# Optimization experiments

Hardware: AMD Instinct MI355X
Metric: run time of the kernel (lower is better)

Reference implementation:

```python
import jax, jax.numpy as jnp
import numpy as np

GROUPS = 32
EPS = 1e-5
NUM_HEADS = 8

def group_norm(x, w, b):
    # x: [B, C, H, W], normalize over (C//G, H, W) per group
    B, C, H, W = x.shape
    xg = x.reshape(B, GROUPS, C // GROUPS, H, W)
    mean = xg.mean(axis=(2, 3, 4), keepdims=True)
    var = xg.var(axis=(2, 3, 4), keepdims=True)
    xg = (xg - mean) * jax.lax.rsqrt(var + EPS)
    x = xg.reshape(B, C, H, W)
    return x * w[None, :, None, None] + b[None, :, None, None]

def setup_inputs() -> dict:
    key = jax.random.key(0)
    ks = jax.random.split(key, 3)
    C = 512
    x = jax.random.normal(ks[0], (8, C, 32, 32), dtype=jnp.float32)
    gn_w = jnp.ones((C,), jnp.float32)
    gn_b = jnp.zeros((C,), jnp.float32)
    # 1x1 conv weights stored as [out, in] matrices
    qkv_w = jax.random.normal(ks[1], (3 * C, C), dtype=jnp.float32) * (C ** -0.5)
    qkv_b = jnp.zeros((3 * C,), jnp.float32)
    proj_w = jax.random.normal(ks[2], (C, C), dtype=jnp.float32) * (C ** -0.5)
    proj_b = jnp.zeros((C,), jnp.float32)
    return {"x": x, "gn_w": gn_w, "gn_b": gn_b, "qkv_w": qkv_w,
            "qkv_b": qkv_b, "proj_w": proj_w, "proj_b": proj_b}

def reference(x, gn_w, gn_b, qkv_w, qkv_b, proj_w, proj_b):
    B, C, H, W = x.shape
    nh = NUM_HEADS
    hd = C // nh
    N = H * W
    residual = x
    xn = group_norm(x, gn_w, gn_b)
    # 1x1 conv == channel matmul: [B, 3C, H, W]
    qkv = jnp.einsum('bchw,oc->bohw', xn, qkv_w) + qkv_b[None, :, None, None]
    # [B, 3, nh, hd, N] -> q/k/v each [B, nh, N, hd]
    qkv = qkv.reshape(B, 3, nh, hd, N).transpose(1, 0, 2, 4, 3)
    q, k, v = qkv[0], qkv[1], qkv[2]
    scale = hd ** -0.5
    attn = jnp.einsum('bhqd,bhkd->bhqk', q, k) * scale
    attn = jax.nn.softmax(attn, axis=-1)
    out = jnp.einsum('bhqk,bhkd->bhqd', attn, v)  # [B, nh, N, hd]
    out = out.transpose(0, 1, 3, 2).reshape(B, C, H, W)
    out = jnp.einsum('bchw,oc->bohw', out, proj_w) + proj_b[None, :, None, None]
    return out + residual
```

## Files before the change

kernel.cpp:

```cpp
#include <hip/hip_runtime.h>


typedef __bf16 bf16;
typedef __bf16 bf16x8 __attribute__((ext_vector_type(8)));
typedef __bf16 bf16x4 __attribute__((ext_vector_type(4)));
typedef float  f32x4  __attribute__((ext_vector_type(4)));

#define MFMA_16x16x32(A, B, C) __builtin_amdgcn_mfma_f32_16x16x32_bf16((A), (B), (C), 0, 0, 0)

static __device__ __forceinline__ void async_stage_128x32(
    const bf16* __restrict__ g0, bf16* lds, int tid) {
  const int wv = tid >> 6, ln = tid & 63;
#pragma unroll
  for (int cc = 0; cc < 2; ++cc) {
    const int c = wv + cc * 4;
    const bf16* g = g0 + (size_t)(c * 16 + (ln >> 2)) * 512 + (ln & 3) * 8;
    __builtin_amdgcn_global_load_lds(
        (const __attribute__((address_space(1))) void*)g,
        (__attribute__((address_space(3))) void*)(lds + c * 512),
        16, 0, 0);
  }
}

__global__ void wconv_kernel(const float* __restrict__ qw, const float* __restrict__ pw,
                             bf16* __restrict__ wq, bf16* __restrict__ wp) {
  const int i = blockIdx.x * 256 + threadIdx.x;
  if (i < 1536 * 512) wq[i] = (bf16)qw[i];
  if (i < 512 * 512)  wp[i] = (bf16)pw[i];
}

__global__ void gn_stats_kernel(const float* __restrict__ x,
                                float* __restrict__ meanp, float* __restrict__ rstdp) {
  const int bg = blockIdx.x;
  const float4* p = (const float4*)(x + (size_t)bg * 16384);
  float s = 0.f, s2 = 0.f;
#pragma unroll 4
  for (int i = threadIdx.x; i < 4096; i += 256) {
    float4 v = p[i];
    s  += (v.x + v.y) + (v.z + v.w);
    s2 += (v.x * v.x + v.y * v.y) + (v.z * v.z + v.w * v.w);
  }
#pragma unroll
  for (int d = 1; d < 64; d <<= 1) {
    s  += __shfl_xor(s,  d);
    s2 += __shfl_xor(s2, d);
  }
  __shared__ float as[4], as2[4];
  if ((threadIdx.x & 63) == 0) { as[threadIdx.x >> 6] = s; as2[threadIdx.x >> 6] = s2; }
  __syncthreads();
  if (threadIdx.x == 0) {
    float S  = as[0] + as[1] + as[2] + as[3];
    float S2 = as2[0] + as2[1] + as2[2] + as2[3];
    float m = S * (1.0f / 16384.0f);
    float v = S2 * (1.0f / 16384.0f) - m * m;
    meanp[bg] = m;
    rstdp[bg] = rsqrtf(v + 1e-5f);
  }
}

__global__ void gn_apply_kernel(const float* __restrict__ x,
                                const float* __restrict__ gn_w, const float* __restrict__ gn_b,
                                const float* __restrict__ meanp, const float* __restrict__ rstdp,
                                bf16* __restrict__ xn_t) {
  const int n0 = blockIdx.x * 64, c0 = blockIdx.y * 64, b = blockIdx.z;
  __shared__ float tile[64 * 68];
  const int t = threadIdx.x;
  const float* xb = x + ((size_t)b * 512 + c0) * 1024 + n0;
#pragma unroll
  for (int i = 0; i < 4; ++i) {
    int idx = t + i * 256;
    int cl  = idx >> 4;
    int n4  = (idx & 15) * 4;
    float4 v = *(const float4*)(xb + (size_t)cl * 1024 + n4);
    int c  = c0 + cl;
    int bg = b * 32 + (c >> 4);
    float sc = rstdp[bg] * gn_w[c];
    float sh = gn_b[c] - meanp[bg] * sc;
    tile[(n4 + 0) * 68 + cl] = v.x * sc + sh;
    tile[(n4 + 1) * 68 + cl] = v.y * sc + sh;
    tile[(n4 + 2) * 68 + cl] = v.z * sc + sh;
    tile[(n4 + 3) * 68 + cl] = v.w * sc + sh;
  }
  __syncthreads();
  bf16* ob = xn_t + ((size_t)b * 1024 + n0) * 512 + c0;
#pragma unroll
  for (int i = 0; i < 16; ++i) {
    int idx = t + i * 256;
    int nl = idx >> 6, cl = idx & 63;
    ob[(size_t)nl * 512 + cl] = (bf16)tile[nl * 68 + cl];
  }
}

__global__ __launch_bounds__(256) void qkv_gemm_kernel(
    const bf16* __restrict__ W, const bf16* __restrict__ xn_t,
    const float* __restrict__ qkv_b, bf16* __restrict__ qkv_t,
    bf16* __restrict__ v_t) {
  const int n0 = blockIdx.x * 128;
  const int o0 = blockIdx.y * 128;
  const int b  = blockIdx.z;
  __shared__ bf16 As[128 * 32];
  __shared__ bf16 Bs[128 * 32];
  const int tid = threadIdx.x, ln = tid & 63, wv = tid >> 6;
  const int mw = (wv >> 1) * 64, nw = (wv & 1) * 64;
  const int l15 = ln & 15, lg = ln >> 4;
  const bf16* gA = W + (size_t)o0 * 512;
  const bf16* gB = xn_t + ((size_t)b * 1024 + n0) * 512;
  f32x4 acc[4][4] = {};
  for (int kk = 0; kk < 512; kk += 32) {
    async_stage_128x32(gA + kk, As, tid);
    async_stage_128x32(gB + kk, Bs, tid);
    __syncthreads();
    bf16x8 af[4], bfr[4];
#pragma unroll
    for (int mi = 0; mi < 4; ++mi)
      af[mi] = *(const bf16x8*)(&As[(mw + mi * 16 + l15) * 32 + lg * 8]);
#pragma unroll
    for (int nj = 0; nj < 4; ++nj)
      bfr[nj] = *(const bf16x8*)(&Bs[(nw + nj * 16 + l15) * 32 + lg * 8]);
#pragma unroll
    for (int mi = 0; mi < 4; ++mi)
#pragma unroll
      for (int nj = 0; nj < 4; ++nj)
        acc[mi][nj] = MFMA_16x16x32(af[mi], bfr[nj], acc[mi][nj]);
    __syncthreads();
  }
  if (o0 < 1024) {
#pragma unroll
    for (int mi = 0; mi < 4; ++mi) {
      const int o = o0 + mw + mi * 16 + lg * 4;
      const float b0 = qkv_b[o], b1 = qkv_b[o + 1], b2 = qkv_b[o + 2], b3 = qkv_b[o + 3];
#pragma unroll
      for (int nj = 0; nj < 4; ++nj) {
        const int n = n0 + nw + nj * 16 + l15;
        f32x4 v = acc[mi][nj];
        bf16x4 st = { (bf16)(v.x + b0), (bf16)(v.y + b1), (bf16)(v.z + b2), (bf16)(v.w + b3) };
        *(bf16x4*)(&qkv_t[((size_t)b * 1024 + n) * 1536 + o]) = st;
      }
    }
  } else {
#pragma unroll
    for (int mi = 0; mi < 4; ++mi) {
      const int o  = o0 + mw + mi * 16 + lg * 4;
      const int hd = o - 1024;
      const float b0 = qkv_b[o], b1 = qkv_b[o + 1], b2 = qkv_b[o + 2], b3 = qkv_b[o + 3];
      bf16* vb = v_t + ((size_t)b * 512 + hd) * 1024;
#pragma unroll
      for (int nj = 0; nj < 4; ++nj) {
        const int n = n0 + nw + nj * 16 + l15;
        f32x4 v = acc[mi][nj];
        vb[0 * 1024 + n] = (bf16)(v.x + b0);
        vb[1 * 1024 + n] = (bf16)(v.y + b1);
        vb[2 * 1024 + n] = (bf16)(v.z + b2);
        vb[3 * 1024 + n] = (bf16)(v.w + b3);
      }
    }
  }
}

__global__ __launch_bounds__(256) void attn_kernel(
    const bf16* __restrict__ qkv_t, const bf16* __restrict__ v_t,
    bf16* __restrict__ at_t) {
  const int qt = blockIdx.x;
  const int b  = blockIdx.y >> 3;
  const int h  = blockIdx.y & 7;
  __shared__ bf16 Kt[64 * 72];
  __shared__ bf16 Vt[64 * 72];
  __shared__ bf16 Pw[4 * 64 * 72];
  const int tid = threadIdx.x, ln = tid & 63, wv = tid >> 6;
  const int l15 = ln & 15, g = ln >> 4;
  const bf16* hq  = qkv_t + (size_t)b * 1024 * 1536 + h * 64;
  const bf16* hk  = hq + 512;
  const bf16* vtb = v_t + (size_t)(b * 8 + h) * 64 * 1024;
  bf16* Pme = &Pw[wv * 64 * 72];

  const int qb = qt * 256 + wv * 64;
  bf16x8 qf[4][2];
#pragma unroll
  for (int m = 0; m < 4; ++m)
#pragma unroll
    for (int ks = 0; ks < 2; ++ks)
      qf[m][ks] = *(const bf16x8*)(hq + (size_t)(qb + m * 16 + l15) * 1536 + ks * 32 + g * 8);

  f32x4 oacc[4][4] = {};
  float mst[4], lst[4];
#pragma unroll
  for (int m = 0; m < 4; ++m) { mst[m] = -1e30f; lst[m] = 0.f; }

  const int srow = tid >> 2, scg = (tid & 3) * 16;
  bf16x8 kpre0 = *(const bf16x8*)(hk + (size_t)srow * 1536 + scg);
  bf16x8 kpre1 = *(const bf16x8*)(hk + (size_t)srow * 1536 + scg + 8);
  bf16x8 vpre0 = *(const bf16x8*)(vtb + (size_t)srow * 1024 + scg);
  bf16x8 vpre1 = *(const bf16x8*)(vtb + (size_t)srow * 1024 + scg + 8);

  for (int kt = 0; kt < 16; ++kt) {
    __syncthreads();
    *(bf16x8*)(&Kt[srow * 72 + scg])     = kpre0;
    *(bf16x8*)(&Kt[srow * 72 + scg + 8]) = kpre1;
    *(bf16x8*)(&Vt[srow * 72 + scg])     = vpre0;
    *(bf16x8*)(&Vt[srow * 72 + scg + 8]) = vpre1;
    __syncthreads();
    if (kt < 15) {
      const bf16* hk2  = hk  + (size_t)((kt + 1) * 64 + srow) * 1536 + scg;
      const bf16* vtb2 = vtb + (size_t)srow * 1024 + (kt + 1) * 64 + scg;
      kpre0 = *(const bf16x8*)(hk2);
      kpre1 = *(const bf16x8*)(hk2 + 8);
      vpre0 = *(const bf16x8*)(vtb2);
      vpre1 = *(const bf16x8*)(vtb2 + 8);
    }

    bf16x8 kf[4][2];
#pragma unroll
    for (int kj = 0; kj < 4; ++kj)
#pragma unroll
      for (int ks = 0; ks < 2; ++ks)
        kf[kj][ks] = *(const bf16x8*)(&Kt[(kj * 16 + l15) * 72 + ks * 32 + g * 8]);

    float alpha[4];
#pragma unroll
    for (int m = 0; m < 4; ++m) {
      f32x4 st[4] = {};
#pragma unroll
      for (int ks = 0; ks < 2; ++ks)
#pragma unroll
        for (int kj = 0; kj < 4; ++kj)
          st[kj] = MFMA_16x16x32(kf[kj][ks], qf[m][ks], st[kj]);
#pragma unroll
      for (int kj = 0; kj < 4; ++kj)
#pragma unroll
        for (int r = 0; r < 4; ++r) st[kj][r] *= 0.125f;
      float mx = st[0][0];
#pragma unroll
      for (int kj = 0; kj < 4; ++kj)
#pragma unroll
        for (int r = 0; r < 4; ++r) mx = fmaxf(mx, st[kj][r]);
      mx = fmaxf(mx, __shfl_xor(mx, 16));
      mx = fmaxf(mx, __shfl_xor(mx, 32));
      const float mnew = fmaxf(mst[m], mx);
      alpha[m] = __expf(mst[m] - mnew);
      mst[m] = mnew;
      float rsum = 0.f;
#pragma unroll
      for (int kj = 0; kj < 4; ++kj) {
        float e0 = __expf(st[kj][0] - mnew);
        float e1 = __expf(st[kj][1] - mnew);
        float e2 = __expf(st[kj][2] - mnew);
        float e3 = __expf(st[kj][3] - mnew);
        rsum += (e0 + e1) + (e2 + e3);
        bf16x4 pe = { (bf16)e0, (bf16)e1, (bf16)e2, (bf16)e3 };
        *(bf16x4*)(&Pme[(m * 16 + l15) * 72 + kj * 16 + g * 4]) = pe;
      }
      lst[m] = lst[m] * alpha[m] + rsum;
#pragma unroll
      for (int dt = 0; dt < 4; ++dt)
#pragma unroll
        for (int r = 0; r < 4; ++r) oacc[m][dt][r] *= alpha[m];
    }

#pragma unroll
    for (int ks = 0; ks < 2; ++ks) {
      bf16x8 vf[4];
#pragma unroll
      for (int dt = 0; dt < 4; ++dt)
        vf[dt] = *(const bf16x8*)(&Vt[(dt * 16 + l15) * 72 + ks * 32 + g * 8]);
#pragma unroll
      for (int m = 0; m < 4; ++m) {
        bf16x8 pf = *(const bf16x8*)(&Pme[(m * 16 + l15) * 72 + ks * 32 + g * 8]);
#pragma unroll
        for (int dt = 0; dt < 4; ++dt)
          oacc[m][dt] = MFMA_16x16x32(vf[dt], pf, oacc[m][dt]);
      }
    }
  }

#pragma unroll
  for (int m = 0; m < 4; ++m) {
    float l = lst[m];
    l += __shfl_xor(l, 16);
    l += __shfl_xor(l, 32);
    const float inv = 1.0f / l;
    const int q = qb + m * 16 + l15;
#pragma unroll
    for (int dt = 0; dt < 4; ++dt) {
      bf16x4 ov = { (bf16)(oacc[m][dt][0] * inv), (bf16)(oacc[m][dt][1] * inv),
                    (bf16)(oacc[m][dt][2] * inv), (bf16)(oacc[m][dt][3] * inv) };
      *(bf16x4*)(&at_t[((size_t)b * 1024 + q) * 512 + h * 64 + dt * 16 + g * 4]) = ov;
    }
  }
}

__global__ __launch_bounds__(256) void proj_gemm_kernel(
    const bf16* __restrict__ at_t, const bf16* __restrict__ wp,
    const float* __restrict__ proj_b, const float* __restrict__ x,
    float* __restrict__ out) {
  const int i0 = blockIdx.x * 128;
  const int c0 = blockIdx.y * 128;
  const int b  = blockIdx.z;
  __shared__ bf16 As[128 * 32];
  __shared__ bf16 Bs[128 * 32];
  const int tid = threadIdx.x, ln = tid & 63, wv = tid >> 6;
  const int mw = (wv >> 1) * 64, nw = (wv & 1) * 64;
  const int l15 = ln & 15, lg = ln >> 4;
  const bf16* gA = at_t + ((size_t)b * 1024 + i0) * 512;
  const bf16* gB = wp + (size_t)c0 * 512;
  f32x4 acc[4][4] = {};
  for (int kk = 0; kk < 512; kk += 32) {
    async_stage_128x32(gA + kk, As, tid);
    async_stage_128x32(gB + kk, Bs, tid);
    __syncthreads();
    bf16x8 af[4], bfr[4];
#pragma unroll
    for (int mi = 0; mi < 4; ++mi)
      af[mi] = *(const bf16x8*)(&As[(mw + mi * 16 + l15) * 32 + lg * 8]);
#pragma unroll
    for (int nj = 0; nj < 4; ++nj)
      bfr[nj] = *(const bf16x8*)(&Bs[(nw + nj * 16 + l15) * 32 + lg * 8]);
#pragma unroll
    for (int mi = 0; mi < 4; ++mi)
#pragma unroll
      for (int nj = 0; nj < 4; ++nj)
        acc[mi][nj] = MFMA_16x16x32(af[mi], bfr[nj], acc[mi][nj]);
    __syncthreads();
  }
#pragma unroll
  for (int mi = 0; mi < 4; ++mi) {
    const int i = i0 + mw + mi * 16 + lg * 4;
#pragma unroll
    for (int nj = 0; nj < 4; ++nj) {
      const int c = c0 + nw + nj * 16 + l15;
      const float bias = proj_b[c];
      const size_t off = ((size_t)b * 512 + c) * 1024 + i;
      const float4 res = *(const float4*)(x + off);
      f32x4 v = acc[mi][nj];
      float4 ov;
      ov.x = v.x + bias + res.x;
      ov.y = v.y + bias + res.y;
      ov.z = v.z + bias + res.z;
      ov.w = v.w + bias + res.w;
      *(float4*)(out + off) = ov;
    }
  }
}

extern "C" void kernel_launch(void* const* d_in, const int* in_sizes, int n_in,
                              void* d_out, int out_size, void* d_ws, size_t ws_size,
                              hipStream_t stream) {
  (void)in_sizes; (void)n_in; (void)out_size; (void)ws_size;
  const float* x      = (const float*)d_in[0];
  const float* gn_w   = (const float*)d_in[1];
  const float* gn_b   = (const float*)d_in[2];
  const float* qkv_w  = (const float*)d_in[3];
  const float* qkv_b  = (const float*)d_in[4];
  const float* proj_w = (const float*)d_in[5];
  const float* proj_b = (const float*)d_in[6];
  float* out = (float*)d_out;

  char* ws = (char*)d_ws;
  float* meanp = (float*)ws;
  float* rstdp = meanp + 256;
  bf16* wq    = (bf16*)(ws + 4096);
  bf16* wp    = wq + (size_t)1536 * 512;
  bf16* xn_t  = wp + (size_t)512 * 512;
  bf16* qkv_t = xn_t + (size_t)8 * 1024 * 512;
  bf16* at_t  = qkv_t + (size_t)8 * 1024 * 1536;
  bf16* v_t   = at_t + (size_t)8 * 1024 * 512;

  hipLaunchKernelGGL(wconv_kernel,    dim3(3072),      dim3(256), 0, stream, qkv_w, proj_w, wq, wp);
  hipLaunchKernelGGL(gn_stats_kernel, dim3(256),       dim3(256), 0, stream, x, meanp, rstdp);
  hipLaunchKernelGGL(gn_apply_kernel, dim3(16, 8, 8),  dim3(256), 0, stream, x, gn_w, gn_b, meanp, rstdp, xn_t);
  hipLaunchKernelGGL(qkv_gemm_kernel, dim3(8, 12, 8),  dim3(256), 0, stream, wq, xn_t, qkv_b, qkv_t, v_t);
  hipLaunchKernelGGL(attn_kernel,     dim3(4, 64),     dim3(256), 0, stream, qkv_t, v_t, at_t);
  hipLaunchKernelGGL(proj_gemm_kernel,dim3(8, 4, 8),   dim3(256), 0, stream, at_t, wp, proj_b, x, out);
}
```

Measured before the change: 174.1 us.

## Split attention KV range across two wave groups and fold softmax scale into Q

The attention kernel now uses 512-thread blocks over twice as many query tiles. Each block's waves split into two halves, each processing half of the key/value sequence with 32 queries per wave, and the partial results are merged through LDS using a log-sum-exp combine. The 1/sqrt(d) scale is applied to Q in the QKV GEMM epilogue rather than to every score tile. The intent is more parallel blocks and fewer registers per wave, so the 256 workgroups fill the GPU better, at the cost of extra LDS traffic and a final merge step.

```diff
diff --git a/kernel.cpp b/kernel.cpp
--- a/kernel.cpp
+++ b/kernel.cpp
@@ -125,6 +125,7 @@
     __syncthreads();
   }
   if (o0 < 1024) {
+    const float qs = (o0 < 512) ? 0.125f : 1.0f;
 #pragma unroll
     for (int mi = 0; mi < 4; ++mi) {
       const int o = o0 + mw + mi * 16 + lg * 4;
@@ -133,7 +134,8 @@
       for (int nj = 0; nj < 4; ++nj) {
         const int n = n0 + nw + nj * 16 + l15;
         f32x4 v = acc[mi][nj];
-        bf16x4 st = { (bf16)(v.x + b0), (bf16)(v.y + b1), (bf16)(v.z + b2), (bf16)(v.w + b3) };
+        bf16x4 st = { (bf16)((v.x + b0) * qs), (bf16)((v.y + b1) * qs),
+                      (bf16)((v.z + b2) * qs), (bf16)((v.w + b3) * qs) };
         *(bf16x4*)(&qkv_t[((size_t)b * 1024 + n) * 1536 + o]) = st;
       }
     }
@@ -157,51 +159,53 @@
   }
 }
 
-__global__ __launch_bounds__(256) void attn_kernel(
+__global__ __launch_bounds__(512, 4) void attn_kernel(
     const bf16* __restrict__ qkv_t, const bf16* __restrict__ v_t,
     bf16* __restrict__ at_t) {
   const int qt = blockIdx.x;
   const int b  = blockIdx.y >> 3;
   const int h  = blockIdx.y & 7;
-  __shared__ bf16 Kt[64 * 72];
-  __shared__ bf16 Vt[64 * 72];
-  __shared__ bf16 Pw[4 * 64 * 72];
+  __shared__ __align__(16) char smem[73728];
   const int tid = threadIdx.x, ln = tid & 63, wv = tid >> 6;
+  const int half = wv >> 2, w4 = wv & 3;
   const int l15 = ln & 15, g = ln >> 4;
+  bf16* Kt = (bf16*)(smem + half * 18432);
+  bf16* Vt = Kt + 64 * 72;
+  bf16* Pme = (bf16*)(smem + 36864) + wv * 32 * 72;
   const bf16* hq  = qkv_t + (size_t)b * 1024 * 1536 + h * 64;
   const bf16* hk  = hq + 512;
   const bf16* vtb = v_t + (size_t)(b * 8 + h) * 64 * 1024;
-  bf16* Pme = &Pw[wv * 64 * 72];
-
-  const int qb = qt * 256 + wv * 64;
-  bf16x8 qf[4][2];
-#pragma unroll
-  for (int m = 0; m < 4; ++m)
+
+  const int qb = qt * 128 + w4 * 32;
+  bf16x8 qf[2][2];
+#pragma unroll
+  for (int m = 0; m < 2; ++m)
 #pragma unroll
     for (int ks = 0; ks < 2; ++ks)
       qf[m][ks] = *(const bf16x8*)(hq + (size_t)(qb + m * 16 + l15) * 1536 + ks * 32 + g * 8);
 
-  f32x4 oacc[4][4] = {};
-  float mst[4], lst[4];
-#pragma unroll
-  for (int m = 0; m < 4; ++m) { mst[m] = -1e30f; lst[m] = 0.f; }
-
-  const int srow = tid >> 2, scg = (tid & 3) * 16;
-  bf16x8 kpre0 = *(const bf16x8*)(hk + (size_t)srow * 1536 + scg);
-  bf16x8 kpre1 = *(const bf16x8*)(hk + (size_t)srow * 1536 + scg + 8);
-  bf16x8 vpre0 = *(const bf16x8*)(vtb + (size_t)srow * 1024 + scg);
-  bf16x8 vpre1 = *(const bf16x8*)(vtb + (size_t)srow * 1024 + scg + 8);
-
-  for (int kt = 0; kt < 16; ++kt) {
+  f32x4 oacc[2][4] = {};
+  float mst[2] = { -1e30f, -1e30f }, lst[2] = { 0.f, 0.f };
+
+  const int t256 = tid & 255;
+  const int srow = t256 >> 2, scg = (t256 & 3) * 16;
+  const int kt0 = half * 8;
+  bf16x8 kpre0 = *(const bf16x8*)(hk + (size_t)(kt0 * 64 + srow) * 1536 + scg);
+  bf16x8 kpre1 = *(const bf16x8*)(hk + (size_t)(kt0 * 64 + srow) * 1536 + scg + 8);
+  bf16x8 vpre0 = *(const bf16x8*)(vtb + (size_t)srow * 1024 + kt0 * 64 + scg);
+  bf16x8 vpre1 = *(const bf16x8*)(vtb + (size_t)srow * 1024 + kt0 * 64 + scg + 8);
+
+  for (int i = 0; i < 8; ++i) {
     __syncthreads();
     *(bf16x8*)(&Kt[srow * 72 + scg])     = kpre0;
     *(bf16x8*)(&Kt[srow * 72 + scg + 8]) = kpre1;
     *(bf16x8*)(&Vt[srow * 72 + scg])     = vpre0;
     *(bf16x8*)(&Vt[srow * 72 + scg + 8]) = vpre1;
     __syncthreads();
-    if (kt < 15) {
-      const bf16* hk2  = hk  + (size_t)((kt + 1) * 64 + srow) * 1536 + scg;
-      const bf16* vtb2 = vtb + (size_t)srow * 1024 + (kt + 1) * 64 + scg;
+    if (i < 7) {
+      const int ktn = kt0 + i + 1;
+      const bf16* hk2  = hk  + (size_t)(ktn * 64 + srow) * 1536 + scg;
+      const bf16* vtb2 = vtb + (size_t)srow * 1024 + ktn * 64 + scg;
       kpre0 = *(const bf16x8*)(hk2);
       kpre1 = *(const bf16x8*)(hk2 + 8);
       vpre0 = *(const bf16x8*)(vtb2);
@@ -215,19 +219,14 @@
       for (int ks = 0; ks < 2; ++ks)
         kf[kj][ks] = *(const bf16x8*)(&Kt[(kj * 16 + l15) * 72 + ks * 32 + g * 8]);
 
-    float alpha[4];
-#pragma unroll
-    for (int m = 0; m < 4; ++m) {
+#pragma unroll
+    for (int m = 0; m < 2; ++m) {
       f32x4 st[4] = {};
 #pragma unroll
       for (int ks = 0; ks < 2; ++ks)
 #pragma unroll
         for (int kj = 0; kj < 4; ++kj)
           st[kj] = MFMA_16x16x32(kf[kj][ks], qf[m][ks], st[kj]);
-#pragma unroll
-      for (int kj = 0; kj < 4; ++kj)
-#pragma unroll
-        for (int r = 0; r < 4; ++r) st[kj][r] *= 0.125f;
       float mx = st[0][0];
 #pragma unroll
       for (int kj = 0; kj < 4; ++kj)
@@ -235,8 +234,8 @@
         for (int r = 0; r < 4; ++r) mx = fmaxf(mx, st[kj][r]);
       mx = fmaxf(mx, __shfl_xor(mx, 16));
       mx = fmaxf(mx, __shfl_xor(mx, 32));
-      const float mnew = fmaxf(mst[m], mx);
-      alpha[m] = __expf(mst[m] - mnew);
+      const float mnew  = fmaxf(mst[m], mx);
+      const float alpha = __expf(mst[m] - mnew);
       mst[m] = mnew;
       float rsum = 0.f;
 #pragma unroll
@@ -249,11 +248,11 @@
         bf16x4 pe = { (bf16)e0, (bf16)e1, (bf16)e2, (bf16)e3 };
         *(bf16x4*)(&Pme[(m * 16 + l15) * 72 + kj * 16 + g * 4]) = pe;
       }
-      lst[m] = lst[m] * alpha[m] + rsum;
+      lst[m] = lst[m] * alpha + rsum;
 #pragma unroll
       for (int dt = 0; dt < 4; ++dt)
 #pragma unroll
-        for (int r = 0; r < 4; ++r) oacc[m][dt][r] *= alpha[m];
+        for (int r = 0; r < 4; ++r) oacc[m][dt][r] *= alpha;
     }
 
 #pragma unroll
@@ -263,7 +262,7 @@
       for (int dt = 0; dt < 4; ++dt)
         vf[dt] = *(const bf16x8*)(&Vt[(dt * 16 + l15) * 72 + ks * 32 + g * 8]);
 #pragma unroll
-      for (int m = 0; m < 4; ++m) {
+      for (int m = 0; m < 2; ++m) {
         bf16x8 pf = *(const bf16x8*)(&Pme[(m * 16 + l15) * 72 + ks * 32 + g * 8]);
 #pragma unroll
         for (int dt = 0; dt < 4; ++dt)
@@ -272,18 +271,52 @@
     }
   }
 
-#pragma unroll
-  for (int m = 0; m < 4; ++m) {
+  float lfull[2];
+#pragma unroll
+  for (int m = 0; m < 2; ++m) {
     float l = lst[m];
     l += __shfl_xor(l, 16);
     l += __shfl_xor(l, 32);
-    const float inv = 1.0f / l;
-    const int q = qb + m * 16 + l15;
-#pragma unroll
-    for (int dt = 0; dt < 4; ++dt) {
-      bf16x4 ov = { (bf16)(oacc[m][dt][0] * inv), (bf16)(oacc[m][dt][1] * inv),
-                    (bf16)(oacc[m][dt][2] * inv), (bf16)(oacc[m][dt][3] * inv) };
-      *(bf16x4*)(&at_t[((size_t)b * 1024 + q) * 512 + h * 64 + dt * 16 + g * 4]) = ov;
+    lfull[m] = l;
+  }
+
+  float* MB  = (float*)smem;
+  float* MLb = (float*)(smem + 36864);
+  __syncthreads();
+  if (half == 1) {
+    float* mb = MB + w4 * (32 * 68);
+#pragma unroll
+    for (int m = 0; m < 2; ++m) {
+#pragma unroll
+      for (int dt = 0; dt < 4; ++dt)
+        *(f32x4*)(mb + (m * 16 + l15) * 68 + dt * 16 + g * 4) = oacc[m][dt];
+      if (g == 0) {
+        MLb[w4 * 64 + (m * 16 + l15)]      = mst[m];
+        MLb[w4 * 64 + 32 + (m * 16 + l15)] = lfull[m];
+      }
+    }
+  }
+  __syncthreads();
+  if (half == 0) {
+    const float* mb = MB + w4 * (32 * 68);
+#pragma unroll
+    for (int m = 0; m < 2; ++m) {
+      const float mB = MLb[w4 * 64 + (m * 16 + l15)];
+      const float lB = MLb[w4 * 64 + 32 + (m * 16 + l15)];
+      const float mM = fmaxf(mst[m], mB);
+      const float ea = __expf(mst[m] - mM);
+      const float eb = __expf(mB - mM);
+      const float inv = 1.0f / (lfull[m] * ea + lB * eb);
+      const int q = qb + m * 16 + l15;
+#pragma unroll
+      for (int dt = 0; dt < 4; ++dt) {
+        f32x4 ob = *(const f32x4*)(mb + (m * 16 + l15) * 68 + dt * 16 + g * 4);
+        bf16x4 ov = { (bf16)((oacc[m][dt][0] * ea + ob[0] * eb) * inv),
+                      (bf16)((oacc[m][dt][1] * ea + ob[1] * eb) * inv),
+                      (bf16)((oacc[m][dt][2] * ea + ob[2] * eb) * inv),
+                      (bf16)((oacc[m][dt][3] * ea + ob[3] * eb) * inv) };
+        *(bf16x4*)(&at_t[((size_t)b * 1024 + q) * 512 + h * 64 + dt * 16 + g * 4]) = ov;
+      }
     }
   }
 }
@@ -368,6 +401,6 @@
   hipLaunchKernelGGL(gn_stats_kernel, dim3(256),       dim3(256), 0, stream, x, meanp, rstdp);
   hipLaunchKernelGGL(gn_apply_kernel, dim3(16, 8, 8),  dim3(256), 0, stream, x, gn_w, gn_b, meanp, rstdp, xn_t);
   hipLaunchKernelGGL(qkv_gemm_kernel, dim3(8, 12, 8),  dim3(256), 0, stream, wq, xn_t, qkv_b, qkv_t, v_t);
-  hipLaunchKernelGGL(attn_kernel,     dim3(4, 64),     dim3(256), 0, stream, qkv_t, v_t, at_t);
+  hipLaunchKernelGGL(attn_kernel,     dim3(8, 64),     dim3(512), 0, stream, qkv_t, v_t, at_t);
   hipLaunchKernelGGL(proj_gemm_kernel,dim3(8, 4, 8),   dim3(256), 0, stream, at_t, wp, proj_b, x, out);
 }
```

Result: no change. 173.3 us (-0.4%).
